# Kernel tuning notes

Hardware: AMD Instinct MI355X
Metric: run time of the kernel (lower is better)

Reference implementation:

```python
import jax, jax.numpy as jnp
import numpy as np

ALPHA = 10.0
K = 10
BN_EPS = 1e-5


def _conv3d(x, w, b, pad):
    # x: [N,C,D,H,W], w: [O,I,kd,kh,kw]
    y = jax.lax.conv_general_dilated(
        x, w, window_strides=(1, 1, 1),
        padding=[(pad, pad)] * 3,
        dimension_numbers=('NCDHW', 'OIDHW', 'NCDHW'))
    return y + b[None, :, None, None, None]


def _bn(x, gamma, beta, mean, var):
    c = (None, slice(None), None, None, None)
    return gamma[c] * (x - mean[c]) * jax.lax.rsqrt(var[c] + BN_EPS) + beta[c]


def setup_inputs() -> dict:
    key = jax.random.key(0)
    ks = jax.random.split(key, 12)
    B, D, H, W = 1, 32, 32, 32
    LAT = 8
    M = 4096  # stored database vectors
    inp = {
        'bg_prob': jax.random.uniform(ks[0], (B, 1, D, H, W), jnp.float32),
        'ed_prob': jax.random.uniform(ks[1], (B, 1, D, H, W), jnp.float32),
        'context_mask': jnp.ones((B, D, H, W), dtype=bool),
        # conv1: 2 -> 16, k3
        'w1': jax.random.normal(ks[2], (16, 2, 3, 3, 3), jnp.float32) * 0.1,
        'b1': jnp.zeros((16,), jnp.float32),
        'g1': jnp.ones((16,), jnp.float32),
        'be1': jnp.zeros((16,), jnp.float32),
        'm1': jnp.zeros((16,), jnp.float32),
        'v1': jnp.ones((16,), jnp.float32),
        # conv2: 16 -> 32, k3
        'w2': jax.random.normal(ks[3], (32, 16, 3, 3, 3), jnp.float32) * 0.05,
        'b2': jnp.zeros((32,), jnp.float32),
        'g2': jnp.ones((32,), jnp.float32),
        'be2': jnp.zeros((32,), jnp.float32),
        'm2': jnp.zeros((32,), jnp.float32),
        'v2': jnp.ones((32,), jnp.float32),
        # conv3: 32 -> latent_dim, k1
        'w3': jax.random.normal(ks[4], (LAT, 32, 1, 1, 1), jnp.float32) * 0.1,
        'b3': jnp.zeros((LAT,), jnp.float32),
    }
    db = jax.random.normal(ks[5], (M, LAT), jnp.float32)
    db = db / jnp.maximum(jnp.linalg.norm(db, axis=1, keepdims=True), 1e-12)
    inp['db_feats'] = db
    inp['db_labels'] = jax.random.uniform(ks[6], (M,), jnp.float32)
    return inp


def reference(bg_prob, ed_prob, context_mask,
              w1, b1, g1, be1, m1, v1,
              w2, b2, g2, be2, m2, v2,
              w3, b3, db_feats, db_labels):
    # --- query encoder (BatchNorm in inference mode) ---
    x = jnp.concatenate([bg_prob, ed_prob], axis=1)              # [B,2,D,H,W]
    x = jax.nn.relu(_bn(_conv3d(x, w1, b1, 1), g1, be1, m1, v1))
    x = jax.nn.relu(_bn(_conv3d(x, w2, b2, 1), g2, be2, m2, v2))
    lat = _conv3d(x, w3, b3, 0)                                   # [B,C,D,H,W]
    # F.normalize(dim=1), eps=1e-12
    lat = lat / jnp.maximum(jnp.linalg.norm(lat, axis=1, keepdims=True), 1e-12)
    B, C, D, H, W = lat.shape
    q = lat.transpose(0, 2, 3, 4, 1).reshape(-1, C)               # [N,C]
    # --- exact L2 kNN (FAISS IndexFlatL2 returns squared distances) ---
    d2 = (jnp.sum(q * q, axis=1, keepdims=True)
          + jnp.sum(db_feats * db_feats, axis=1)[None, :]
          - 2.0 * q @ db_feats.T)                                 # [N,M]
    neg_top, idx = jax.lax.top_k(-d2, K)                          # k smallest
    dists = -neg_top                                              # [N,K]
    w = jnp.exp(-ALPHA * dists)
    lbl = db_labels[idx]                                          # [N,K] gather
    pred = jnp.sum(w * lbl, axis=1) / (jnp.sum(w, axis=1) + 1e-8)
    # NOTE: original view(B,2,D,H,W) is inconsistent (N=B*D*H*W preds);
    # return the consistent [B,D,H,W].
    return pred.reshape(B, D, H, W)
```

## Files before the change

### kernel.cpp

```cpp
#include <hip/hip_runtime.h>

#define ALPHA 10.0f
#define BN_EPS 1e-5f
#define NVOX 32768
#define MDB 4096
#define CAP 128

typedef __attribute__((ext_vector_type(8))) short short8;
typedef __attribute__((ext_vector_type(16))) float f32x16;

__device__ __forceinline__ unsigned short bfr(float x) {
  unsigned u = __float_as_uint(x);
  return (unsigned short)((u + 0x7FFFu + ((u >> 16) & 1u)) >> 16);
}
__device__ __forceinline__ void split3(float x, unsigned short& h,
                                       unsigned short& m, unsigned short& l) {
  h = bfr(x);
  float fh = __uint_as_float((unsigned)h << 16);
  float x1 = x - fh;
  m = bfr(x1);
  float fm = __uint_as_float((unsigned)m << 16);
  l = bfr(x1 - fm);
}

__device__ __forceinline__ f32x16 d2_tile(short8 a1, short8 a2, short8 a3,
                                          short8 a4, short8 b1, short8 b3,
                                          short8 b4) {
  f32x16 acc = {};
  acc = __builtin_amdgcn_mfma_f32_32x32x16_bf16(a4, b4, acc, 0, 0, 0);
  acc = __builtin_amdgcn_mfma_f32_32x32x16_bf16(a3, b3, acc, 0, 0, 0);
  acc = __builtin_amdgcn_mfma_f32_32x32x16_bf16(a2, b1, acc, 0, 0, 0);
  acc = __builtin_amdgcn_mfma_f32_32x32x16_bf16(a1, b1, acc, 0, 0, 0);
  return acc;
}

__device__ __forceinline__ float fmin3(float a, float b, float c) {
  return fminf(fminf(a, b), c);
}

#define INSERT2(d, va, vb)                                              \
  do {                                                                  \
    float _lo = fminf((va), (vb)), _hi = fmaxf((va), (vb));             \
    _Pragma("unroll")                                                   \
    for (int _k = 9; _k >= 2; --_k)                                     \
      d[_k] = fmin3(d[_k], fmaxf(d[_k - 1], _lo), fmaxf(d[_k - 2], _hi)); \
    d[1] = fmin3(d[1], fmaxf(d[0], _lo), _hi);                          \
    d[0] = fminf(d[0], _lo);                                            \
  } while (0)

__global__ __launch_bounds__(256) void k_conv1p(
    const float* __restrict__ bg, const float* __restrict__ ed,
    const float* __restrict__ w1, const float* __restrict__ b1,
    const float* __restrict__ g1, const float* __restrict__ be1,
    const float* __restrict__ m1, const float* __restrict__ v1,
    float* __restrict__ A, const float* __restrict__ db,
    unsigned short* __restrict__ DBH, unsigned short* __restrict__ DBM,
    unsigned short* __restrict__ DBL, unsigned short* __restrict__ DB4) {
  int t = threadIdx.x;
  if (blockIdx.x >= 128) {
    int j = (blockIdx.x - 128) * 256 + t;
    float4 x0 = ((const float4*)(db + (size_t)j * 8))[0];
    float4 x1 = ((const float4*)(db + (size_t)j * 8))[1];
    float x[8] = {x0.x, x0.y, x0.z, x0.w, x1.x, x1.y, x1.z, x1.w};
    float ss = x[0] * x[0];
#pragma unroll
    for (int i = 1; i < 8; ++i) ss = fmaf(x[i], x[i], ss);
    short8 sh = {}, sm = {}, sl = {};
#pragma unroll
    for (int i = 0; i < 8; ++i) {
      unsigned short h, m, l;
      split3(-2.f * x[i], h, m, l);
      sh[i] = (short)h; sm[i] = (short)m; sl[i] = (short)l;
    }
    unsigned short dh, dm, dl;
    split3(ss, dh, dm, dl);
    short8 s4 = {};
    s4[0] = (short)dh; s4[1] = (short)dm; s4[2] = (short)dl;
    s4[3] = (short)0x3F80; s4[4] = (short)0x3F80; s4[5] = (short)0x3F80;
    *(short8*)(DBH + (size_t)j * 8) = sh;
    *(short8*)(DBM + (size_t)j * 8) = sm;
    *(short8*)(DBL + (size_t)j * 8) = sl;
    *(short8*)(DB4 + (size_t)j * 8) = s4;
    return;
  }
  __shared__ float wT[54 * 16];
  __shared__ float sc[16], shs[16];
  for (int i = t; i < 864; i += 256) {
    int o = i & 15, r = i >> 4;
    wT[i] = w1[o * 54 + r];
  }
  if (t < 16) {
    float s = g1[t] * rsqrtf(v1[t] + BN_EPS);
    sc[t] = s;
    shs[t] = (b1[t] - m1[t]) * s + be1[t];
  }
  __syncthreads();
  int v = blockIdx.x * 256 + t;
  int x = v & 31, y = (v >> 5) & 31, z = v >> 10;
  float acc[16];
#pragma unroll
  for (int o = 0; o < 16; ++o) acc[o] = 0.f;
#pragma unroll 1
  for (int k = 0; k < 27; ++k) {
    int dz = k / 9 - 1, dy = (k / 3) % 3 - 1, dx = k % 3 - 1;
    int zz = z + dz, yy = y + dy, xx = x + dx;
    bool inb = (unsigned)zz < 32u && (unsigned)yy < 32u && (unsigned)xx < 32u;
    int vv = zz * 1024 + yy * 32 + xx;
#pragma unroll
    for (int c = 0; c < 2; ++c) {
      const float* in = c ? ed : bg;
      float val = inb ? in[vv] : 0.f;
      const float4* wp = (const float4*)&wT[(c * 27 + k) * 16];
      float4 wa = wp[0], wb = wp[1], wc = wp[2], wd = wp[3];
      acc[0] = fmaf(val, wa.x, acc[0]);  acc[1] = fmaf(val, wa.y, acc[1]);
      acc[2] = fmaf(val, wa.z, acc[2]);  acc[3] = fmaf(val, wa.w, acc[3]);
      acc[4] = fmaf(val, wb.x, acc[4]);  acc[5] = fmaf(val, wb.y, acc[5]);
      acc[6] = fmaf(val, wb.z, acc[6]);  acc[7] = fmaf(val, wb.w, acc[7]);
      acc[8] = fmaf(val, wc.x, acc[8]);  acc[9] = fmaf(val, wc.y, acc[9]);
      acc[10] = fmaf(val, wc.z, acc[10]); acc[11] = fmaf(val, wc.w, acc[11]);
      acc[12] = fmaf(val, wd.x, acc[12]); acc[13] = fmaf(val, wd.y, acc[13]);
      acc[14] = fmaf(val, wd.z, acc[14]); acc[15] = fmaf(val, wd.w, acc[15]);
    }
  }
#pragma unroll
  for (int o = 0; o < 16; ++o) {
    float y2 = fmaf(acc[o], sc[o], shs[o]);
    A[o * NVOX + v] = y2 > 0.f ? y2 : 0.f;
  }
}

__global__ __launch_bounds__(256) void k_conv2(
    const float* __restrict__ A, const float* __restrict__ w2,
    const float* __restrict__ b2, const float* __restrict__ g2,
    const float* __restrict__ be2, const float* __restrict__ m2,
    const float* __restrict__ v2, float* __restrict__ B) {
  __shared__ float wT[432 * 8];
  __shared__ float sc[8], shs[8];
  int t = threadIdx.x;
  int og = blockIdx.x >> 7;
  int vb = blockIdx.x & 127;
  for (int i = t; i < 3456; i += 256) {
    int o = i & 7, r = i >> 3;
    wT[i] = w2[(og * 8 + o) * 432 + r];
  }
  if (t < 8) {
    int o = og * 8 + t;
    float s = g2[o] * rsqrtf(v2[o] + BN_EPS);
    sc[t] = s;
    shs[t] = (b2[o] - m2[o]) * s + be2[o];
  }
  __syncthreads();
  int v = vb * 256 + t;
  int x = v & 31, y = (v >> 5) & 31, z = v >> 10;
  float acc[8];
#pragma unroll
  for (int o = 0; o < 8; ++o) acc[o] = 0.f;
#pragma unroll 1
  for (int k = 0; k < 27; ++k) {
    int dz = k / 9 - 1, dy = (k / 3) % 3 - 1, dx = k % 3 - 1;
    int zz = z + dz, yy = y + dy, xx = x + dx;
    bool inb = (unsigned)zz < 32u && (unsigned)yy < 32u && (unsigned)xx < 32u;
    int vv = zz * 1024 + yy * 32 + xx;
#pragma unroll
    for (int ci = 0; ci < 16; ++ci) {
      float val = inb ? A[ci * NVOX + vv] : 0.f;
      const float4* wp = (const float4*)&wT[(ci * 27 + k) * 8];
      float4 wa = wp[0], wb = wp[1];
      acc[0] = fmaf(val, wa.x, acc[0]); acc[1] = fmaf(val, wa.y, acc[1]);
      acc[2] = fmaf(val, wa.z, acc[2]); acc[3] = fmaf(val, wa.w, acc[3]);
      acc[4] = fmaf(val, wb.x, acc[4]); acc[5] = fmaf(val, wb.y, acc[5]);
      acc[6] = fmaf(val, wb.z, acc[6]); acc[7] = fmaf(val, wb.w, acc[7]);
    }
  }
#pragma unroll
  for (int o = 0; o < 8; ++o) {
    float y2 = fmaf(acc[o], sc[o], shs[o]);
    B[(og * 8 + o) * NVOX + v] = y2 > 0.f ? y2 : 0.f;
  }
}

__global__ __launch_bounds__(512) void k_knn_fused(
    const float* __restrict__ B, const float* __restrict__ w3,
    const float* __restrict__ b3c,
    const unsigned short* __restrict__ DBH, const unsigned short* __restrict__ DBM,
    const unsigned short* __restrict__ DBL, const unsigned short* __restrict__ DB4,
    const float* __restrict__ labels, float* __restrict__ out) {
  __shared__ float smem[2 * 32 * (CAP + 1)];
  __shared__ float T0L[32];
  __shared__ int cnt[32];
  __shared__ float pn[32][16];
  __shared__ float wTl[256];
  __shared__ float bLl[8];
  float (*listd)[CAP + 1] = (float (*)[CAP + 1])smem;
  int (*listi)[CAP + 1] = (int (*)[CAP + 1])(smem + 32 * (CAP + 1));
  float (*lds_top)[10][32] = (float (*)[10][32])smem;

  int t = threadIdx.x, w = t >> 6, l = t & 63;
  int lo32 = l & 31, hi = l >> 5;
  if (t < 32) cnt[t] = 0;
  if (t < 256) wTl[t] = w3[(t & 7) * 32 + (t >> 3)];
  if (t >= 504) bLl[t - 504] = b3c[t - 504];
  __syncthreads();

  short8 zz = {};
  short8 b1, b3, b4;
  {
    int v = blockIdx.x * 32 + lo32;
    float lat[8];
#pragma unroll
    for (int o = 0; o < 8; ++o) lat[o] = bLl[o];
#pragma unroll 4
    for (int ci = 0; ci < 32; ++ci) {
      float val = B[(size_t)ci * NVOX + v];
      const float4* wp = (const float4*)&wTl[ci * 8];
      float4 wa = wp[0], wb = wp[1];
      lat[0] = fmaf(val, wa.x, lat[0]); lat[1] = fmaf(val, wa.y, lat[1]);
      lat[2] = fmaf(val, wa.z, lat[2]); lat[3] = fmaf(val, wa.w, lat[3]);
      lat[4] = fmaf(val, wb.x, lat[4]); lat[5] = fmaf(val, wb.y, lat[5]);
      lat[6] = fmaf(val, wb.z, lat[6]); lat[7] = fmaf(val, wb.w, lat[7]);
    }
    float n2 = 0.f;
#pragma unroll
    for (int o = 0; o < 8; ++o) n2 = fmaf(lat[o], lat[o], n2);
    float inv = 1.f / fmaxf(sqrtf(n2), 1e-12f);
    float qv[8];
#pragma unroll
    for (int o = 0; o < 8; ++o) qv[o] = lat[o] * inv;
    float qq2 = qv[0] * qv[0];
#pragma unroll
    for (int o = 1; o < 8; ++o) qq2 = fmaf(qv[o], qv[o], qq2);
    short8 sh = {}, sm = {}, sl = {};
#pragma unroll
    for (int o = 0; o < 8; ++o) {
      unsigned short h, m, lo;
      split3(qv[o], h, m, lo);
      sh[o] = (short)h; sm[o] = (short)m; sl[o] = (short)lo;
    }
    unsigned short qh, qm, ql;
    split3(qq2, qh, qm, ql);
    short8 s4 = {};
    s4[0] = (short)0x3F80; s4[1] = (short)0x3F80; s4[2] = (short)0x3F80;
    s4[3] = (short)qh; s4[4] = (short)qm; s4[5] = (short)ql;
    b1 = hi ? sm : sh;
    b3 = hi ? sl : sh;
    b4 = hi ? zz : s4;
  }
  int r0 = w * 512;

  float d[10];
#pragma unroll
  for (int k = 0; k < 10; ++k) d[k] = 3.4e38f;
#pragma unroll 1
  for (int tt = 0; tt < 3; ++tt) {
    int r = r0 + tt * 32 + lo32;
    short8 a1 = *(const short8*)(DBH + (size_t)r * 8);
    short8 a2 = *(const short8*)(DBM + (size_t)r * 8);
    short8 a3 = *(const short8*)((hi ? DBH : DBL) + (size_t)r * 8);
    short8 a4 = *(const short8*)(DB4 + (size_t)r * 8);
    f32x16 acc = d2_tile(a1, a2, a3, a4, b1, b3, b4);
#pragma unroll
    for (int p = 0; p < 8; ++p) INSERT2(d, acc[2 * p], acc[2 * p + 1]);
  }
  {
    float e[10];
#pragma unroll
    for (int k = 0; k < 10; ++k) e[k] = __shfl_xor(d[k], 32);
#pragma unroll
    for (int k = 0; k < 10; k += 2) INSERT2(d, e[k], e[k + 1]);
  }
  if (l < 32) {
#pragma unroll
    for (int k = 0; k < 10; ++k) lds_top[w][k][lo32] = d[k];
  }
  __syncthreads();
  if (t < 32) {
    float m[10];
#pragma unroll
    for (int k = 0; k < 10; ++k) m[k] = 3.4e38f;
#pragma unroll 1
    for (int w2 = 0; w2 < 8; ++w2) {
#pragma unroll
      for (int k2 = 0; k2 < 10; k2 += 2)
        INSERT2(m, lds_top[w2][k2][t], lds_top[w2][k2 + 1][t]);
    }
    T0L[t] = m[9];
  }
  __syncthreads();
  float T0q = T0L[lo32];

#pragma unroll 1
  for (int tt = 0; tt < 16; ++tt) {
    int r = r0 + tt * 32 + lo32;
    short8 a1 = *(const short8*)(DBH + (size_t)r * 8);
    short8 a2 = *(const short8*)(DBM + (size_t)r * 8);
    short8 a3 = *(const short8*)((hi ? DBH : DBL) + (size_t)r * 8);
    short8 a4 = *(const short8*)(DB4 + (size_t)r * 8);
    f32x16 acc = d2_tile(a1, a2, a3, a4, b1, b3, b4);
    int rb = r0 + tt * 32 + 4 * hi;
#pragma unroll
    for (int i = 0; i < 16; ++i) {
      float d2v = acc[i];
      if (d2v <= T0q) {
        int slot = atomicAdd(&cnt[lo32], 1);
        if (slot < CAP) {
          listd[lo32][slot] = d2v;
          listi[lo32][slot] = rb + (i & 3) + 8 * (i >> 2);
        }
      }
    }
  }
  __syncthreads();

  float den = 0.f;
  if (t < 32) {
    int n = min(cnt[t], CAP);
    float dd[10];
#pragma unroll
    for (int k = 0; k < 10; ++k) dd[k] = 3.4e38f;
    int j = 0;
#pragma unroll 1
    for (; j + 1 < n; j += 2) INSERT2(dd, listd[t][j], listd[t][j + 1]);
    if (j < n) INSERT2(dd, listd[t][j], 3.4e38f);
    const float C2 = -14.4269504088896340736f;
#pragma unroll
    for (int k = 0; k < 10; ++k) den += exp2f(dd[k] * C2);
    T0L[t] = dd[9];
  }
  __syncthreads();

  {
    const float C2 = -14.4269504088896340736f;
    int qc = t >> 4, s0 = t & 15;
    int n = min(cnt[qc], CAP);
    float Tq = T0L[qc];
    float nump = 0.f;
    for (int s = s0; s < n; s += 16) {
      float v = listd[qc][s];
      if (v <= Tq) nump = fmaf(exp2f(v * C2), labels[listi[qc][s]], nump);
    }
    pn[qc][s0] = nump;
  }
  __syncthreads();
  if (t < 32) {
    float num = 0.f;
#pragma unroll
    for (int g = 0; g < 16; ++g) num += pn[t][g];
    out[blockIdx.x * 32 + t] = num / (den + 1e-8f);
  }
}

extern "C" void kernel_launch(void* const* d_in, const int* in_sizes, int n_in,
                              void* d_out, int out_size, void* d_ws, size_t ws_size,
                              hipStream_t stream) {
  const float* bg = (const float*)d_in[0];
  const float* ed = (const float*)d_in[1];
  const float* w1 = (const float*)d_in[3];
  const float* b1 = (const float*)d_in[4];
  const float* g1 = (const float*)d_in[5];
  const float* be1 = (const float*)d_in[6];
  const float* m1 = (const float*)d_in[7];
  const float* v1 = (const float*)d_in[8];
  const float* w2 = (const float*)d_in[9];
  const float* b2 = (const float*)d_in[10];
  const float* g2 = (const float*)d_in[11];
  const float* be2 = (const float*)d_in[12];
  const float* m2 = (const float*)d_in[13];
  const float* v2 = (const float*)d_in[14];
  const float* w3 = (const float*)d_in[15];
  const float* b3 = (const float*)d_in[16];
  const float* db = (const float*)d_in[17];
  const float* labels = (const float*)d_in[18];
  float* out = (float*)d_out;

  char* ws = (char*)d_ws;
  const size_t MB = 1024 * 1024;
  float* A = (float*)(ws + 0);
  float* B = (float*)(ws + 2 * MB);
  unsigned short* DBH = (unsigned short*)(ws + 6 * MB);
  unsigned short* DBM = DBH + (size_t)MDB * 8;
  unsigned short* DBL = DBM + (size_t)MDB * 8;
  unsigned short* DB4 = DBL + (size_t)MDB * 8;

  k_conv1p<<<144, 256, 0, stream>>>(bg, ed, w1, b1, g1, be1, m1, v1, A, db,
                                    DBH, DBM, DBL, DB4);
  k_conv2<<<4 * 128, 256, 0, stream>>>(A, w2, b2, g2, be2, m2, v2, B);
  k_knn_fused<<<NVOX / 32, 512, 0, stream>>>(B, w3, b3, DBH, DBM, DBL, DB4,
                                             labels, out);
}
```

Before: 107.5 us.

## Fuse conv2 into the kNN kernel using an LDS halo tile per row

Removes the separate conv2 kernel. Each kNN block, which covers one 32-voxel row, now loads a 16x3x3x34 halo of conv1 output into shared memory and computes all 32 conv2 channels for its row: 512 threads, two output channels each. The result stays in LDS and feeds the 1x1 latent conv directly. This drops a launch and the global round trip of the 32-channel intermediate. In exchange, halo voxels are loaded redundantly across blocks and the conv2 weights are read straight from global memory in the inner loop rather than staged in LDS.

```diff
diff --git a/kernel.cpp b/kernel.cpp
--- a/kernel.cpp
+++ b/kernel.cpp
@@ -129,58 +129,11 @@
   }
 }
 
-__global__ __launch_bounds__(256) void k_conv2(
+__global__ __launch_bounds__(512) void k_knn_fused(
     const float* __restrict__ A, const float* __restrict__ w2,
     const float* __restrict__ b2, const float* __restrict__ g2,
     const float* __restrict__ be2, const float* __restrict__ m2,
-    const float* __restrict__ v2, float* __restrict__ B) {
-  __shared__ float wT[432 * 8];
-  __shared__ float sc[8], shs[8];
-  int t = threadIdx.x;
-  int og = blockIdx.x >> 7;
-  int vb = blockIdx.x & 127;
-  for (int i = t; i < 3456; i += 256) {
-    int o = i & 7, r = i >> 3;
-    wT[i] = w2[(og * 8 + o) * 432 + r];
-  }
-  if (t < 8) {
-    int o = og * 8 + t;
-    float s = g2[o] * rsqrtf(v2[o] + BN_EPS);
-    sc[t] = s;
-    shs[t] = (b2[o] - m2[o]) * s + be2[o];
-  }
-  __syncthreads();
-  int v = vb * 256 + t;
-  int x = v & 31, y = (v >> 5) & 31, z = v >> 10;
-  float acc[8];
-#pragma unroll
-  for (int o = 0; o < 8; ++o) acc[o] = 0.f;
-#pragma unroll 1
-  for (int k = 0; k < 27; ++k) {
-    int dz = k / 9 - 1, dy = (k / 3) % 3 - 1, dx = k % 3 - 1;
-    int zz = z + dz, yy = y + dy, xx = x + dx;
-    bool inb = (unsigned)zz < 32u && (unsigned)yy < 32u && (unsigned)xx < 32u;
-    int vv = zz * 1024 + yy * 32 + xx;
-#pragma unroll
-    for (int ci = 0; ci < 16; ++ci) {
-      float val = inb ? A[ci * NVOX + vv] : 0.f;
-      const float4* wp = (const float4*)&wT[(ci * 27 + k) * 8];
-      float4 wa = wp[0], wb = wp[1];
-      acc[0] = fmaf(val, wa.x, acc[0]); acc[1] = fmaf(val, wa.y, acc[1]);
-      acc[2] = fmaf(val, wa.z, acc[2]); acc[3] = fmaf(val, wa.w, acc[3]);
-      acc[4] = fmaf(val, wb.x, acc[4]); acc[5] = fmaf(val, wb.y, acc[5]);
-      acc[6] = fmaf(val, wb.z, acc[6]); acc[7] = fmaf(val, wb.w, acc[7]);
-    }
-  }
-#pragma unroll
-  for (int o = 0; o < 8; ++o) {
-    float y2 = fmaf(acc[o], sc[o], shs[o]);
-    B[(og * 8 + o) * NVOX + v] = y2 > 0.f ? y2 : 0.f;
-  }
-}
-
-__global__ __launch_bounds__(512) void k_knn_fused(
-    const float* __restrict__ B, const float* __restrict__ w3,
+    const float* __restrict__ v2, const float* __restrict__ w3,
     const float* __restrict__ b3c,
     const unsigned short* __restrict__ DBH, const unsigned short* __restrict__ DBM,
     const unsigned short* __restrict__ DBL, const unsigned short* __restrict__ DB4,
@@ -194,24 +147,66 @@
   float (*listd)[CAP + 1] = (float (*)[CAP + 1])smem;
   int (*listi)[CAP + 1] = (int (*)[CAP + 1])(smem + 32 * (CAP + 1));
   float (*lds_top)[10][32] = (float (*)[10][32])smem;
+  float* AH = smem;
+  float* C2 = smem + 4896;
 
   int t = threadIdx.x, w = t >> 6, l = t & 63;
   int lo32 = l & 31, hi = l >> 5;
   if (t < 32) cnt[t] = 0;
   if (t < 256) wTl[t] = w3[(t & 7) * 32 + (t >> 3)];
   if (t >= 504) bLl[t - 504] = b3c[t - 504];
-  __syncthreads();
-
-  short8 zz = {};
-  short8 b1, b3, b4;
+
+  int y0 = blockIdx.x & 31, z0 = blockIdx.x >> 5;
+
+  for (int i = t; i < 4896; i += 512) {
+    int xi = i % 34;
+    int rest = i / 34;
+    int yi = rest % 3;
+    rest /= 3;
+    int zi = rest % 3;
+    int ci = rest / 3;
+    int xx = xi - 1, yy = y0 + yi - 1, zz = z0 + zi - 1;
+    bool inb = (unsigned)xx < 32u && (unsigned)yy < 32u && (unsigned)zz < 32u;
+    AH[i] = inb ? A[(size_t)ci * NVOX + zz * 1024 + yy * 32 + xx] : 0.f;
+  }
+  __syncthreads();
+
   {
-    int v = blockIdx.x * 32 + lo32;
+    int x = t & 31;
+    int oc0 = t >> 5, oc1 = oc0 + 16;
+    float acc0 = 0.f, acc1 = 0.f;
+#pragma unroll 1
+    for (int k = 0; k < 27; ++k) {
+      int kz = k / 9, ky = (k / 3) % 3, kx = k % 3;
+      int base = kz * 102 + ky * 34 + x + kx;
+#pragma unroll
+      for (int ci = 0; ci < 16; ++ci) {
+        float val = AH[ci * 306 + base];
+        acc0 = fmaf(val, w2[(size_t)oc0 * 432 + ci * 27 + k], acc0);
+        acc1 = fmaf(val, w2[(size_t)oc1 * 432 + ci * 27 + k], acc1);
+      }
+    }
+    float s0 = g2[oc0] * rsqrtf(v2[oc0] + BN_EPS);
+    float h0 = (b2[oc0] - m2[oc0]) * s0 + be2[oc0];
+    float s1 = g2[oc1] * rsqrtf(v2[oc1] + BN_EPS);
+    float h1 = (b2[oc1] - m2[oc1]) * s1 + be2[oc1];
+    float r0 = fmaf(acc0, s0, h0);
+    float r1 = fmaf(acc1, s1, h1);
+    __syncthreads();
+    C2[oc0 * 32 + x] = r0 > 0.f ? r0 : 0.f;
+    C2[oc1 * 32 + x] = r1 > 0.f ? r1 : 0.f;
+  }
+  __syncthreads();
+
+  short8 zz8 = {};
+  short8 b1f, b3f, b4f;
+  {
     float lat[8];
 #pragma unroll
     for (int o = 0; o < 8; ++o) lat[o] = bLl[o];
 #pragma unroll 4
     for (int ci = 0; ci < 32; ++ci) {
-      float val = B[(size_t)ci * NVOX + v];
+      float val = C2[ci * 32 + lo32];
       const float4* wp = (const float4*)&wTl[ci * 8];
       float4 wa = wp[0], wb = wp[1];
       lat[0] = fmaf(val, wa.x, lat[0]); lat[1] = fmaf(val, wa.y, lat[1]);
@@ -241,10 +236,11 @@
     short8 s4 = {};
     s4[0] = (short)0x3F80; s4[1] = (short)0x3F80; s4[2] = (short)0x3F80;
     s4[3] = (short)qh; s4[4] = (short)qm; s4[5] = (short)ql;
-    b1 = hi ? sm : sh;
-    b3 = hi ? sl : sh;
-    b4 = hi ? zz : s4;
-  }
+    b1f = hi ? sm : sh;
+    b3f = hi ? sl : sh;
+    b4f = hi ? zz8 : s4;
+  }
+  __syncthreads();
   int r0 = w * 512;
 
   float d[10];
@@ -257,7 +253,7 @@
     short8 a2 = *(const short8*)(DBM + (size_t)r * 8);
     short8 a3 = *(const short8*)((hi ? DBH : DBL) + (size_t)r * 8);
     short8 a4 = *(const short8*)(DB4 + (size_t)r * 8);
-    f32x16 acc = d2_tile(a1, a2, a3, a4, b1, b3, b4);
+    f32x16 acc = d2_tile(a1, a2, a3, a4, b1f, b3f, b4f);
 #pragma unroll
     for (int p = 0; p < 8; ++p) INSERT2(d, acc[2 * p], acc[2 * p + 1]);
   }
@@ -278,10 +274,10 @@
 #pragma unroll
     for (int k = 0; k < 10; ++k) m[k] = 3.4e38f;
 #pragma unroll 1
-    for (int w2 = 0; w2 < 8; ++w2) {
+    for (int w2i = 0; w2i < 8; ++w2i) {
 #pragma unroll
       for (int k2 = 0; k2 < 10; k2 += 2)
-        INSERT2(m, lds_top[w2][k2][t], lds_top[w2][k2 + 1][t]);
+        INSERT2(m, lds_top[w2i][k2][t], lds_top[w2i][k2 + 1][t]);
     }
     T0L[t] = m[9];
   }
@@ -295,7 +291,7 @@
     short8 a2 = *(const short8*)(DBM + (size_t)r * 8);
     short8 a3 = *(const short8*)((hi ? DBH : DBL) + (size_t)r * 8);
     short8 a4 = *(const short8*)(DB4 + (size_t)r * 8);
-    f32x16 acc = d2_tile(a1, a2, a3, a4, b1, b3, b4);
+    f32x16 acc = d2_tile(a1, a2, a3, a4, b1f, b3f, b4f);
     int rb = r0 + tt * 32 + 4 * hi;
 #pragma unroll
     for (int i = 0; i < 16; ++i) {
@@ -321,22 +317,22 @@
 #pragma unroll 1
     for (; j + 1 < n; j += 2) INSERT2(dd, listd[t][j], listd[t][j + 1]);
     if (j < n) INSERT2(dd, listd[t][j], 3.4e38f);
-    const float C2 = -14.4269504088896340736f;
-#pragma unroll
-    for (int k = 0; k < 10; ++k) den += exp2f(dd[k] * C2);
+    const float C2c = -14.4269504088896340736f;
+#pragma unroll
+    for (int k = 0; k < 10; ++k) den += exp2f(dd[k] * C2c);
     T0L[t] = dd[9];
   }
   __syncthreads();
 
   {
-    const float C2 = -14.4269504088896340736f;
+    const float C2c = -14.4269504088896340736f;
     int qc = t >> 4, s0 = t & 15;
     int n = min(cnt[qc], CAP);
     float Tq = T0L[qc];
     float nump = 0.f;
     for (int s = s0; s < n; s += 16) {
       float v = listd[qc][s];
-      if (v <= Tq) nump = fmaf(exp2f(v * C2), labels[listi[qc][s]], nump);
+      if (v <= Tq) nump = fmaf(exp2f(v * C2c), labels[listi[qc][s]], nump);
     }
     pn[qc][s0] = nump;
   }
@@ -375,7 +371,6 @@
   char* ws = (char*)d_ws;
   const size_t MB = 1024 * 1024;
   float* A = (float*)(ws + 0);
-  float* B = (float*)(ws + 2 * MB);
   unsigned short* DBH = (unsigned short*)(ws + 6 * MB);
   unsigned short* DBM = DBH + (size_t)MDB * 8;
   unsigned short* DBL = DBM + (size_t)MDB * 8;
@@ -383,7 +378,7 @@
 
   k_conv1p<<<144, 256, 0, stream>>>(bg, ed, w1, b1, g1, be1, m1, v1, A, db,
                                     DBH, DBM, DBL, DB4);
-  k_conv2<<<4 * 128, 256, 0, stream>>>(A, w2, b2, g2, be2, m2, v2, B);
-  k_knn_fused<<<NVOX / 32, 512, 0, stream>>>(B, w3, b3, DBH, DBM, DBL, DB4,
-                                             labels, out);
-}
+  k_knn_fused<<<NVOX / 32, 512, 0, stream>>>(A, w2, b2, g2, be2, m2, v2, w3,
+                                             b3, DBH, DBM, DBL, DB4, labels,
+                                             out);
+}
```

New measurement: 124.5 us. 1.16x slower.
